# Performance work log

Measured on AMD Instinct MI355X. Metric: run time of the kernel, lower is better.

The kernel has to match this reference:

```python
import jax, jax.numpy as jnp
import numpy as np

B, T, C, HS = 4, 4096, 1024, 128

def setup_inputs() -> dict:
    key = jax.random.key(0)
    kx, kk, kq, kv = jax.random.split(key, 4)
    x = jax.random.normal(kx, (B, T, C), dtype=jnp.float32)
    # torch Linear(n_embd, head_size, bias=False): y = x @ W.T with W [hs, C].
    # We store the transposed form W [C, hs] so y = x @ W (same math).
    s = C ** -0.5  # kaiming-ish scale to keep activations sane
    Wk = jax.random.normal(kk, (C, HS), dtype=jnp.float32) * s
    Wq = jax.random.normal(kq, (C, HS), dtype=jnp.float32) * s
    Wv = jax.random.normal(kv, (C, HS), dtype=jnp.float32) * s
    return {"x": x, "Wk": Wk, "Wq": Wq, "Wv": Wv}

def reference(x, Wk, Wq, Wv):
    # Single causal self-attention head (dropout = identity, eval mode).
    k = jnp.einsum('btc,ch->bth', x, Wk)  # [B,T,hs]
    q = jnp.einsum('btc,ch->bth', x, Wq)
    v = jnp.einsum('btc,ch->bth', x, Wv)
    scale = k.shape[-1] ** -0.5
    wei = jnp.einsum('bqh,bkh->bqk', q, k) * scale  # [B,T,T]
    Tq = x.shape[1]
    causal = jnp.tril(jnp.ones((Tq, Tq), dtype=bool))
    wei = jnp.where(causal, wei, -jnp.inf)
    wei = jax.nn.softmax(wei, axis=-1)
    out = jnp.einsum('bqk,bkh->bqh', wei, v)  # [B,T,hs]
    return out
```

## Files before the change

kernel.cpp:

```cpp
#include <hip/hip_runtime.h>
#include <hip/hip_bf16.h>
#include <math.h>

#define B_  4
#define T_  4096
#define C_  1024
#define HS_ 128

using bf16x8 = __attribute__((ext_vector_type(8))) __bf16;
using bf16x4 = __attribute__((ext_vector_type(4))) __bf16;
using f32x4  = __attribute__((ext_vector_type(4))) float;

#define MFMA(a, b, c) __builtin_amdgcn_mfma_f32_16x16x32_bf16(a, b, c, 0, 0, 0)

typedef __attribute__((address_space(1))) const float gfloat;
typedef __attribute__((address_space(3))) float lfloat;

__device__ inline float fexp2(float x) {
  float r;
  asm volatile("v_exp_f32 %0, %1\n\ts_nop 0" : "=v"(r) : "v"(x));
  return r;
}


__global__ __launch_bounds__(256) void prep_w_kernel(
    const float* __restrict__ Wk, const float* __restrict__ Wq,
    const float* __restrict__ Wv, __bf16* __restrict__ Wt) {
  const int m  = blockIdx.x >> 4;
  const int k0 = (blockIdx.x & 15) * 64;
  const float* W = (m == 0) ? Wq : ((m == 1) ? Wk : Wv);
  const float scale = (m == 0) ? (0.08838834764831845f * 1.4426950408889634f) : 1.0f;
  __shared__ __bf16 tile[128][72];
  const int t = threadIdx.x;
#pragma unroll
  for (int p = 0; p < 8; ++p) {
    int e  = p * 1024 + t * 4;
    int r  = e >> 7;
    int cc = e & 127;
    float4 w = *reinterpret_cast<const float4*>(&W[(size_t)(k0 + r) * HS_ + cc]);
    tile[cc + 0][r] = (__bf16)(w.x * scale);
    tile[cc + 1][r] = (__bf16)(w.y * scale);
    tile[cc + 2][r] = (__bf16)(w.z * scale);
    tile[cc + 3][r] = (__bf16)(w.w * scale);
  }
  __syncthreads();
#pragma unroll
  for (int p = 0; p < 4; ++p) {
    int e  = p * 2048 + t * 8;
    int n  = e >> 6;
    int kk = e & 63;
    bf16x8 v;
#pragma unroll
    for (int jj = 0; jj < 8; ++jj) v[jj] = tile[n][kk + jj];
    *reinterpret_cast<bf16x8*>(&Wt[((size_t)m * 128 + n) * C_ + k0 + kk]) = v;
  }
}

__device__ inline bf16x8 cvt8p(float4 u, float4 v) {
  bf16x8 r;
  r[0] = (__bf16)u.x; r[1] = (__bf16)u.y; r[2] = (__bf16)u.z; r[3] = (__bf16)u.w;
  r[4] = (__bf16)v.x; r[5] = (__bf16)v.y; r[6] = (__bf16)v.z; r[7] = (__bf16)v.w;
  return r;
}

__global__ __launch_bounds__(256) void proj_kernel(
    const float* __restrict__ x, const __bf16* __restrict__ Wt,
    __bf16* __restrict__ Qf, __bf16* __restrict__ Kf, __bf16* __restrict__ Vf) {
  __shared__ __align__(16) char lds[57344];
  const int tid = threadIdx.x;
  const int wid = tid >> 6;
  const int l   = tid & 63;
  const int c   = l & 15;
  const int g   = l >> 4;
  const int rbase = blockIdx.x * 32;

  f32x4 acc[6][2];
#pragma unroll
  for (int i = 0; i < 6; ++i) { acc[i][0] = 0.f; acc[i][1] = 0.f; }

  const int xrow = tid >> 3;
  const int xch  = tid & 7;
  const float* xsrc = x + (size_t)(rbase + xrow) * C_ + ((xch ^ (xrow & 7)) << 2);
  const __bf16* wsrc[6];
#pragma unroll
  for (int i = 0; i < 6; ++i) {
    int id2 = i * 256 + tid;
    int cg  = id2 >> 2;
    int kc  = id2 & 3;
    wsrc[i] = Wt + (size_t)cg * C_ + ((kc ^ (cg & 3)) << 3);
  }

  auto stage = [&](int t, int bo) {
    __builtin_amdgcn_global_load_lds((gfloat*)(xsrc + t * 32),
        (lfloat*)(lds + bo + tid * 16), 16, 0, 0);
#pragma unroll
    for (int i = 0; i < 6; ++i)
      __builtin_amdgcn_global_load_lds((gfloat*)(wsrc[i] + t * 32),
          (lfloat*)(lds + bo + 4096 + (i * 256 + tid) * 16), 16, 0, 0);
  };

  int woffs[6];
#pragma unroll
  for (int i = 0; i < 6; ++i) {
    int u  = wid * 6 + i;
    int cg = (u >> 3) * 128 + (u & 7) * 16 + c;
    woffs[i] = 4096 + cg * 64 + ((g ^ (cg & 3)) << 4);
  }
  int xoffs[2][2];
#pragma unroll
  for (int rt = 0; rt < 2; ++rt) {
    int row = rt * 16 + c;
#pragma unroll
    for (int j = 0; j < 2; ++j)
      xoffs[rt][j] = row * 128 + ((((g << 1) | j) ^ (row & 7)) << 4);
  }

  stage(0, 0);
  asm volatile("s_waitcnt vmcnt(0)" ::: "memory");
  __syncthreads();

  for (int t = 0; t < 32; ++t) {
    const int bo = (t & 1) * 28672;
    if (t + 1 < 32) stage(t + 1, bo ^ 28672);

    bf16x8 wf[6];
#pragma unroll
    for (int i = 0; i < 6; ++i)
      wf[i] = *reinterpret_cast<const bf16x8*>(lds + bo + woffs[i]);
#pragma unroll
    for (int rt = 0; rt < 2; ++rt) {
      float4 lo = *reinterpret_cast<const float4*>(lds + bo + xoffs[rt][0]);
      float4 hi = *reinterpret_cast<const float4*>(lds + bo + xoffs[rt][1]);
      bf16x8 a = cvt8p(lo, hi);
#pragma unroll
      for (int i = 0; i < 6; ++i) acc[i][rt] = MFMA(a, wf[i], acc[i][rt]);
    }

    asm volatile("s_waitcnt vmcnt(0)" ::: "memory");
    __syncthreads();
  }

  const size_t tile = blockIdx.x;
#pragma unroll
  for (int i = 0; i < 6; ++i) {
    const int u = wid * 6 + i;
    const int m = u >> 3, nt = u & 7;
    const int gprime = ((nt & 1) << 1) + (c >> 3);
    const int e = c & 7;
    if (m == 0) {
#pragma unroll
      for (int rt = 0; rt < 2; ++rt)
#pragma unroll
        for (int rr = 0; rr < 4; ++rr)
          Qf[(tile * 8 + rt * 4 + (nt >> 1)) * 512 +
             (gprime * 16 + 4 * g + rr) * 8 + e] = (__bf16)acc[i][rt][rr];
    } else if (m == 1) {
#pragma unroll
      for (int rt = 0; rt < 2; ++rt)
#pragma unroll
        for (int rr = 0; rr < 4; ++rr)
          Kf[(tile * 8 + 2 * (nt >> 1) + (g & 1)) * 512 +
             (gprime * 16 + (((2 * rt + (g >> 1)) << 2) | rr)) * 8 + e] =
              (__bf16)acc[i][rt][rr];
    } else {
#pragma unroll
      for (int rt = 0; rt < 2; ++rt) {
        bf16x4 v4;
#pragma unroll
        for (int rr = 0; rr < 4; ++rr) v4[rr] = (__bf16)acc[i][rt][rr];
        *reinterpret_cast<bf16x4*>(
            Vf + (tile * 8 + nt) * 512 +
            ((2 * rt + (g >> 1)) * 16 + c) * 8 + 4 * (g & 1)) = v4;
      }
    }
  }
}

__global__ __launch_bounds__(256, 2) void attn_kernel(
    const __bf16* __restrict__ Qf, const __bf16* __restrict__ Kf,
    const __bf16* __restrict__ Vf, float* __restrict__ out) {
  __shared__ float sm[4][32];
  __shared__ float sl[4][32];
  __shared__ float bufA[32][132];
  __shared__ float bufB[32][132];

  const int tid = threadIdx.x;
  const int wid = tid >> 6;
  const int l   = tid & 63;
  const int c   = l & 15;
  const int g   = l >> 4;
  const int bid = blockIdx.x;
  const int b   = (bid & 7) >> 1;
  const int j   = ((bid >> 3) << 1) | (bid & 1);
  const int qt  = (j < 64) ? (127 - j) : (j - 64);
  const int qb  = qt * 32;

  bf16x8 qf[2][4];
  {
    const __bf16* Qt = Qf + (size_t)(b * 128 + qt) * 4096 + l * 8;
#pragma unroll
    for (int rt = 0; rt < 2; ++rt)
#pragma unroll
      for (int cs = 0; cs < 4; ++cs)
        qf[rt][cs] = *reinterpret_cast<const bf16x8*>(Qt + (rt * 4 + cs) * 512);
  }

  f32x4 acc[2][8];
#pragma unroll
  for (int i = 0; i < 2; ++i)
#pragma unroll
    for (int d = 0; d < 8; ++d) acc[i][d] = 0.f;
  float mrun[2] = {-INFINITY, -INFINITY};
  float lrun[2] = {0.f, 0.f};

  if (wid <= qt) {
    const __bf16* Kb8 = Kf + (size_t)b * 128 * 4096 + l * 8;
    const __bf16* Vb8 = Vf + (size_t)b * 128 * 4096 + l * 8;
    bf16x8 kreg[8];
    auto kload = [&](int kt) {
      const __bf16* kb = Kb8 + (size_t)kt * 4096;
#pragma unroll
      for (int jj = 0; jj < 8; ++jj)
        kreg[jj] = *reinterpret_cast<const bf16x8*>(kb + jj * 512);
    };
    kload(wid);

    for (int kt = wid; kt <= qt; kt += 4) {
      f32x4 s00 = 0.f, s01 = 0.f, s10 = 0.f, s11 = 0.f;
      __builtin_amdgcn_s_setprio(1);
#pragma unroll
      for (int cs = 0; cs < 4; ++cs) {
        s00 = MFMA(kreg[2 * cs], qf[0][cs], s00);
        s01 = MFMA(kreg[2 * cs + 1], qf[0][cs], s01);
        s10 = MFMA(kreg[2 * cs], qf[1][cs], s10);
        s11 = MFMA(kreg[2 * cs + 1], qf[1][cs], s11);
      }
      __builtin_amdgcn_s_setprio(0);

      bf16x8 vf[8];
      {
        const __bf16* vb = Vb8 + (size_t)kt * 4096;
#pragma unroll
        for (int db = 0; db < 8; ++db)
          vf[db] = *reinterpret_cast<const bf16x8*>(vb + db * 512);
      }

      if (kt + 4 <= qt) kload(kt + 4);

      const bool maskt = (kt == qt);
      bf16x8 pb[2];
#pragma unroll
      for (int rt = 0; rt < 2; ++rt) {
        float p[8];
        const f32x4 sa = rt ? s10 : s00;
        const f32x4 sb = rt ? s11 : s01;
#pragma unroll
        for (int rr = 0; rr < 4; ++rr) { p[rr] = sa[rr]; p[4 + rr] = sb[rr]; }
        if (maskt) {
          const int lim = rt * 16 + c;
#pragma unroll
          for (int jj = 0; jj < 8; ++jj)
            if (8 * g + jj > lim) p[jj] = -INFINITY;
        }
        float t0 = fmaxf(fmaxf(p[0], p[1]), p[2]);
        float t1 = fmaxf(fmaxf(p[3], p[4]), p[5]);
        float t2 = fmaxf(fmaxf(p[6], p[7]), t0);
        float tmax = fmaxf(t1, t2);

        if (!__all(tmax <= mrun[rt] + 11.5415603f)) {
          float cmax = fmaxf(tmax, __shfl_xor(tmax, 16));
          cmax = fmaxf(cmax, __shfl_xor(cmax, 32));
          float mnew = fmaxf(mrun[rt], cmax);
          float al   = fexp2(mrun[rt] - mnew);
          mrun[rt] = mnew;
          lrun[rt] *= al;
#pragma unroll
          for (int db = 0; db < 8; ++db) acc[rt][db] *= al;
        }
        const float mc = mrun[rt];
#pragma unroll
        for (int jj = 0; jj < 8; ++jj) p[jj] = fexp2(p[jj] - mc);
        lrun[rt] += ((p[0] + p[1]) + (p[2] + p[3])) + ((p[4] + p[5]) + (p[6] + p[7]));
#pragma unroll
        for (int jj = 0; jj < 8; ++jj) pb[rt][jj] = (__bf16)p[jj];
      }

      __builtin_amdgcn_s_setprio(1);
#pragma unroll
      for (int db = 0; db < 8; ++db) {
        acc[0][db] = MFMA(vf[db], pb[0], acc[0][db]);
        acc[1][db] = MFMA(vf[db], pb[1], acc[1][db]);
      }
      __builtin_amdgcn_s_setprio(0);
    }
  }

#pragma unroll
  for (int rt = 0; rt < 2; ++rt) {
    lrun[rt] += __shfl_xor(lrun[rt], 16);
    lrun[rt] += __shfl_xor(lrun[rt], 32);
  }

  if (g == 0) {
    sm[wid][c] = mrun[0]; sm[wid][16 + c] = mrun[1];
    sl[wid][c] = lrun[0]; sl[wid][16 + c] = lrun[1];
  }
  __syncthreads();

  float linv[2];
#pragma unroll
  for (int rt = 0; rt < 2; ++rt) {
    const int q = rt * 16 + c;
    float ms = fmaxf(fmaxf(sm[0][q], sm[1][q]), fmaxf(sm[2][q], sm[3][q]));
    float ls = fexp2(sm[0][q] - ms) * sl[0][q] + fexp2(sm[1][q] - ms) * sl[1][q]
             + fexp2(sm[2][q] - ms) * sl[2][q] + fexp2(sm[3][q] - ms) * sl[3][q];
    float al = fexp2(mrun[rt] - ms);
#pragma unroll
    for (int db = 0; db < 8; ++db) acc[rt][db] *= al;
    linv[rt] = 1.0f / ls;
  }

  auto store_buf = [&](float(*buf)[132]) {
#pragma unroll
    for (int rt = 0; rt < 2; ++rt)
#pragma unroll
      for (int db = 0; db < 8; ++db)
        *reinterpret_cast<f32x4*>(&buf[rt * 16 + c][db * 16 + 4 * g]) = acc[rt][db];
  };
  auto add_buf = [&](float(*buf)[132]) {
#pragma unroll
    for (int rt = 0; rt < 2; ++rt)
#pragma unroll
      for (int db = 0; db < 8; ++db)
        acc[rt][db] += *reinterpret_cast<const f32x4*>(&buf[rt * 16 + c][db * 16 + 4 * g]);
  };

  if (wid == 2) store_buf(bufA);
  if (wid == 3) store_buf(bufB);
  __syncthreads();
  if (wid == 0) add_buf(bufA);
  if (wid == 1) add_buf(bufB);
  __syncthreads();
  if (wid == 1) store_buf(bufA);
  __syncthreads();
  if (wid == 0) {
    add_buf(bufA);
    float* op = out + ((size_t)b * T_ + qb) * HS_;
#pragma unroll
    for (int rt = 0; rt < 2; ++rt)
#pragma unroll
      for (int db = 0; db < 8; ++db) {
        f32x4 v = acc[rt][db] * linv[rt];
        *reinterpret_cast<f32x4*>(op + (size_t)(rt * 16 + c) * HS_ + db * 16 + 4 * g) = v;
      }
  }
}

extern "C" void kernel_launch(void* const* d_in, const int* in_sizes, int n_in,
                              void* d_out, int out_size, void* d_ws, size_t ws_size,
                              hipStream_t stream) {
  const float* x  = (const float*)d_in[0];
  const float* Wk = (const float*)d_in[1];
  const float* Wq = (const float*)d_in[2];
  const float* Wv = (const float*)d_in[3];
  float* out = (float*)d_out;

  char* ws = (char*)d_ws;
  __bf16* Wt = (__bf16*)ws;
  __bf16* Qf = (__bf16*)(ws + 786432);
  __bf16* Kf = (__bf16*)(ws + 786432 + 4194304);
  __bf16* Vf = (__bf16*)(ws + 786432 + 8388608);

  prep_w_kernel<<<48, 256, 0, stream>>>(Wk, Wq, Wv, Wt);
  proj_kernel<<<512, 256, 0, stream>>>(x, Wt, Qf, Kf, Vf);
  attn_kernel<<<512, 256, 0, stream>>>(Qf, Kf, Vf, out);
}
```

Before: 72.42 us.

## Pre-swizzle weights into MFMA fragment order and load projection operands directly to registers

The weight-prep kernel now writes the bf16 weights in a fragment-major layout that matches the MFMA B-operand. The projection kernel drops its LDS double buffer and barriers and loads x and W fragments straight from global memory into registers, prefetching one k-step ahead. This removes LDS traffic and block-level synchronisation. In exchange each wave reads x rows redundantly from global or L2, and register pressure rises from holding the prefetched fragments.

```diff
diff --git a/kernel.cpp b/kernel.cpp
--- a/kernel.cpp
+++ b/kernel.cpp
@@ -13,9 +13,6 @@
 
 #define MFMA(a, b, c) __builtin_amdgcn_mfma_f32_16x16x32_bf16(a, b, c, 0, 0, 0)
 
-typedef __attribute__((address_space(1))) const float gfloat;
-typedef __attribute__((address_space(3))) float lfloat;
-
 __device__ inline float fexp2(float x) {
   float r;
   asm volatile("v_exp_f32 %0, %1\n\ts_nop 0" : "=v"(r) : "v"(x));
@@ -25,7 +22,7 @@
 
 __global__ __launch_bounds__(256) void prep_w_kernel(
     const float* __restrict__ Wk, const float* __restrict__ Wq,
-    const float* __restrict__ Wv, __bf16* __restrict__ Wt) {
+    const float* __restrict__ Wv, __bf16* __restrict__ Wf) {
   const int m  = blockIdx.x >> 4;
   const int k0 = (blockIdx.x & 15) * 64;
   const float* W = (m == 0) ? Wq : ((m == 1) ? Wk : Wv);
@@ -52,7 +49,11 @@
     bf16x8 v;
 #pragma unroll
     for (int jj = 0; jj < 8; ++jj) v[jj] = tile[n][kk + jj];
-    *reinterpret_cast<bf16x8*>(&Wt[((size_t)m * 128 + n) * C_ + k0 + kk]) = v;
+    int u  = m * 8 + (n >> 4);
+    int ts = (k0 + kk) >> 5;
+    int g2 = (kk >> 3) & 3;
+    *reinterpret_cast<bf16x8*>(
+        &Wf[((size_t)(u * 32 + ts) * 64 + g2 * 16 + (n & 15)) * 8]) = v;
   }
 }
 
@@ -64,9 +65,8 @@
 }
 
 __global__ __launch_bounds__(256) void proj_kernel(
-    const float* __restrict__ x, const __bf16* __restrict__ Wt,
+    const float* __restrict__ x, const __bf16* __restrict__ Wf,
     __bf16* __restrict__ Qf, __bf16* __restrict__ Kf, __bf16* __restrict__ Vf) {
-  __shared__ __align__(16) char lds[57344];
   const int tid = threadIdx.x;
   const int wid = tid >> 6;
   const int l   = tid & 63;
@@ -78,66 +78,45 @@
 #pragma unroll
   for (int i = 0; i < 6; ++i) { acc[i][0] = 0.f; acc[i][1] = 0.f; }
 
-  const int xrow = tid >> 3;
-  const int xch  = tid & 7;
-  const float* xsrc = x + (size_t)(rbase + xrow) * C_ + ((xch ^ (xrow & 7)) << 2);
-  const __bf16* wsrc[6];
-#pragma unroll
-  for (int i = 0; i < 6; ++i) {
-    int id2 = i * 256 + tid;
-    int cg  = id2 >> 2;
-    int kc  = id2 & 3;
-    wsrc[i] = Wt + (size_t)cg * C_ + ((kc ^ (cg & 3)) << 3);
-  }
-
-  auto stage = [&](int t, int bo) {
-    __builtin_amdgcn_global_load_lds((gfloat*)(xsrc + t * 32),
-        (lfloat*)(lds + bo + tid * 16), 16, 0, 0);
+  const float*  xb = x + (size_t)(rbase + c) * C_ + g * 8;
+  const __bf16* wb = Wf + (size_t)(wid * 6) * 16384 + l * 8;
+
+  float4 xc[4], xn[4];
+  bf16x8 wc[6], wn[6];
+
+  auto xload = [&](float4* d, int t) {
+    const float* p0 = xb + t * 32;
+    d[0] = *reinterpret_cast<const float4*>(p0);
+    d[1] = *reinterpret_cast<const float4*>(p0 + 4);
+    d[2] = *reinterpret_cast<const float4*>(p0 + 16 * C_);
+    d[3] = *reinterpret_cast<const float4*>(p0 + 16 * C_ + 4);
+  };
+  auto wload = [&](bf16x8* d, int t) {
 #pragma unroll
     for (int i = 0; i < 6; ++i)
-      __builtin_amdgcn_global_load_lds((gfloat*)(wsrc[i] + t * 32),
-          (lfloat*)(lds + bo + 4096 + (i * 256 + tid) * 16), 16, 0, 0);
+      d[i] = *reinterpret_cast<const bf16x8*>(wb + i * 16384 + t * 512);
   };
 
-  int woffs[6];
-#pragma unroll
-  for (int i = 0; i < 6; ++i) {
-    int u  = wid * 6 + i;
-    int cg = (u >> 3) * 128 + (u & 7) * 16 + c;
-    woffs[i] = 4096 + cg * 64 + ((g ^ (cg & 3)) << 4);
-  }
-  int xoffs[2][2];
-#pragma unroll
-  for (int rt = 0; rt < 2; ++rt) {
-    int row = rt * 16 + c;
-#pragma unroll
-    for (int j = 0; j < 2; ++j)
-      xoffs[rt][j] = row * 128 + ((((g << 1) | j) ^ (row & 7)) << 4);
-  }
-
-  stage(0, 0);
-  asm volatile("s_waitcnt vmcnt(0)" ::: "memory");
-  __syncthreads();
+  xload(xc, 0);
+  wload(wc, 0);
 
   for (int t = 0; t < 32; ++t) {
-    const int bo = (t & 1) * 28672;
-    if (t + 1 < 32) stage(t + 1, bo ^ 28672);
-
-    bf16x8 wf[6];
-#pragma unroll
-    for (int i = 0; i < 6; ++i)
-      wf[i] = *reinterpret_cast<const bf16x8*>(lds + bo + woffs[i]);
-#pragma unroll
-    for (int rt = 0; rt < 2; ++rt) {
-      float4 lo = *reinterpret_cast<const float4*>(lds + bo + xoffs[rt][0]);
-      float4 hi = *reinterpret_cast<const float4*>(lds + bo + xoffs[rt][1]);
-      bf16x8 a = cvt8p(lo, hi);
-#pragma unroll
-      for (int i = 0; i < 6; ++i) acc[i][rt] = MFMA(a, wf[i], acc[i][rt]);
+    if (t + 1 < 32) { xload(xn, t + 1); wload(wn, t + 1); }
+
+    bf16x8 a0 = cvt8p(xc[0], xc[1]);
+    bf16x8 a1 = cvt8p(xc[2], xc[3]);
+#pragma unroll
+    for (int i = 0; i < 6; ++i) {
+      acc[i][0] = MFMA(a0, wc[i], acc[i][0]);
+      acc[i][1] = MFMA(a1, wc[i], acc[i][1]);
     }
 
-    asm volatile("s_waitcnt vmcnt(0)" ::: "memory");
-    __syncthreads();
+    if (t + 1 < 32) {
+#pragma unroll
+      for (int j = 0; j < 4; ++j) xc[j] = xn[j];
+#pragma unroll
+      for (int i = 0; i < 6; ++i) wc[i] = wn[i];
+    }
   }
 
   const size_t tile = blockIdx.x;
@@ -366,12 +345,12 @@
   float* out = (float*)d_out;
 
   char* ws = (char*)d_ws;
-  __bf16* Wt = (__bf16*)ws;
+  __bf16* Wf = (__bf16*)ws;
   __bf16* Qf = (__bf16*)(ws + 786432);
   __bf16* Kf = (__bf16*)(ws + 786432 + 4194304);
   __bf16* Vf = (__bf16*)(ws + 786432 + 8388608);
 
-  prep_w_kernel<<<48, 256, 0, stream>>>(Wk, Wq, Wv, Wt);
-  proj_kernel<<<512, 256, 0, stream>>>(x, Wt, Qf, Kf, Vf);
+  prep_w_kernel<<<48, 256, 0, stream>>>(Wk, Wq, Wv, Wf);
+  proj_kernel<<<512, 256, 0, stream>>>(x, Wf, Qf, Kf, Vf);
   attn_kernel<<<512, 256, 0, stream>>>(Qf, Kf, Vf, out);
 }
```

Measured after the change: 77.90 us. 1.08x slower.

## Pre-swizzle weights into MFMA fragment layout and double proj block to 512 threads

Applied to the files above, without the earlier changes.

The weight prep kernel now writes bf16 weights directly in per-tile MFMA fragment order, so each 32-wide k-step of a 16-column tile is one contiguous 1KB chunk. The projection kernel uses 512 threads (8 waves), each wave handling 3 output tiles instead of 6. This halves per-wave accumulators and loads and makes weight staging fully contiguous, with no XOR swizzle. The x tile is staged by only the first 256 threads. The aim is more waves to hide latency and simpler, coalesced weight loads, at the cost of reading the shared x fragment twice as many times across waves.

```diff
diff --git a/kernel.cpp b/kernel.cpp
--- a/kernel.cpp
+++ b/kernel.cpp
@@ -25,7 +25,7 @@
 
 __global__ __launch_bounds__(256) void prep_w_kernel(
     const float* __restrict__ Wk, const float* __restrict__ Wq,
-    const float* __restrict__ Wv, __bf16* __restrict__ Wt) {
+    const float* __restrict__ Wv, __bf16* __restrict__ Wf) {
   const int m  = blockIdx.x >> 4;
   const int k0 = (blockIdx.x & 15) * 64;
   const float* W = (m == 0) ? Wq : ((m == 1) ? Wk : Wv);
@@ -52,7 +52,11 @@
     bf16x8 v;
 #pragma unroll
     for (int jj = 0; jj < 8; ++jj) v[jj] = tile[n][kk + jj];
-    *reinterpret_cast<bf16x8*>(&Wt[((size_t)m * 128 + n) * C_ + k0 + kk]) = v;
+    int u  = m * 8 + (n >> 4);
+    int ts = (k0 + kk) >> 5;
+    int g2 = (kk >> 3) & 3;
+    *reinterpret_cast<bf16x8*>(
+        &Wf[((size_t)(u * 32 + ts) * 64 + g2 * 16 + (n & 15)) * 8]) = v;
   }
 }
 
@@ -63,8 +67,8 @@
   return r;
 }
 
-__global__ __launch_bounds__(256) void proj_kernel(
-    const float* __restrict__ x, const __bf16* __restrict__ Wt,
+__global__ __launch_bounds__(512) void proj_kernel(
+    const float* __restrict__ x, const __bf16* __restrict__ Wf,
     __bf16* __restrict__ Qf, __bf16* __restrict__ Kf, __bf16* __restrict__ Vf) {
   __shared__ __align__(16) char lds[57344];
   const int tid = threadIdx.x;
@@ -74,38 +78,38 @@
   const int g   = l >> 4;
   const int rbase = blockIdx.x * 32;
 
-  f32x4 acc[6][2];
-#pragma unroll
-  for (int i = 0; i < 6; ++i) { acc[i][0] = 0.f; acc[i][1] = 0.f; }
-
-  const int xrow = tid >> 3;
+  f32x4 acc[3][2];
+#pragma unroll
+  for (int i = 0; i < 3; ++i) { acc[i][0] = 0.f; acc[i][1] = 0.f; }
+
+  const int xrow = (tid & 255) >> 3;
   const int xch  = tid & 7;
   const float* xsrc = x + (size_t)(rbase + xrow) * C_ + ((xch ^ (xrow & 7)) << 2);
-  const __bf16* wsrc[6];
-#pragma unroll
-  for (int i = 0; i < 6; ++i) {
-    int id2 = i * 256 + tid;
-    int cg  = id2 >> 2;
-    int kc  = id2 & 3;
-    wsrc[i] = Wt + (size_t)cg * C_ + ((kc ^ (cg & 3)) << 3);
+  const __bf16* wsrc[3];
+  int wdst[3];
+#pragma unroll
+  for (int i = 0; i < 3; ++i) {
+    int id = i * 512 + tid;
+    int u  = id >> 6;
+    int ln = id & 63;
+    wsrc[i] = Wf + (size_t)u * 32 * 512 + ln * 8;
+    wdst[i] = 4096 + id * 16;
   }
 
   auto stage = [&](int t, int bo) {
-    __builtin_amdgcn_global_load_lds((gfloat*)(xsrc + t * 32),
-        (lfloat*)(lds + bo + tid * 16), 16, 0, 0);
-#pragma unroll
-    for (int i = 0; i < 6; ++i)
-      __builtin_amdgcn_global_load_lds((gfloat*)(wsrc[i] + t * 32),
-          (lfloat*)(lds + bo + 4096 + (i * 256 + tid) * 16), 16, 0, 0);
+    if (tid < 256)
+      __builtin_amdgcn_global_load_lds((gfloat*)(xsrc + t * 32),
+          (lfloat*)(lds + bo + tid * 16), 16, 0, 0);
+#pragma unroll
+    for (int i = 0; i < 3; ++i)
+      __builtin_amdgcn_global_load_lds((gfloat*)(wsrc[i] + t * 512),
+          (lfloat*)(lds + bo + wdst[i]), 16, 0, 0);
   };
 
-  int woffs[6];
-#pragma unroll
-  for (int i = 0; i < 6; ++i) {
-    int u  = wid * 6 + i;
-    int cg = (u >> 3) * 128 + (u & 7) * 16 + c;
-    woffs[i] = 4096 + cg * 64 + ((g ^ (cg & 3)) << 4);
-  }
+  int woffs[3];
+#pragma unroll
+  for (int i = 0; i < 3; ++i)
+    woffs[i] = 4096 + (wid * 3 + i) * 1024 + l * 16;
   int xoffs[2][2];
 #pragma unroll
   for (int rt = 0; rt < 2; ++rt) {
@@ -123,9 +127,9 @@
     const int bo = (t & 1) * 28672;
     if (t + 1 < 32) stage(t + 1, bo ^ 28672);
 
-    bf16x8 wf[6];
-#pragma unroll
-    for (int i = 0; i < 6; ++i)
+    bf16x8 wf[3];
+#pragma unroll
+    for (int i = 0; i < 3; ++i)
       wf[i] = *reinterpret_cast<const bf16x8*>(lds + bo + woffs[i]);
 #pragma unroll
     for (int rt = 0; rt < 2; ++rt) {
@@ -133,7 +137,7 @@
       float4 hi = *reinterpret_cast<const float4*>(lds + bo + xoffs[rt][1]);
       bf16x8 a = cvt8p(lo, hi);
 #pragma unroll
-      for (int i = 0; i < 6; ++i) acc[i][rt] = MFMA(a, wf[i], acc[i][rt]);
+      for (int i = 0; i < 3; ++i) acc[i][rt] = MFMA(a, wf[i], acc[i][rt]);
     }
 
     asm volatile("s_waitcnt vmcnt(0)" ::: "memory");
@@ -142,8 +146,8 @@
 
   const size_t tile = blockIdx.x;
 #pragma unroll
-  for (int i = 0; i < 6; ++i) {
-    const int u = wid * 6 + i;
+  for (int i = 0; i < 3; ++i) {
+    const int u = wid * 3 + i;
     const int m = u >> 3, nt = u & 7;
     const int gprime = ((nt & 1) << 1) + (c >> 3);
     const int e = c & 7;
@@ -366,12 +370,12 @@
   float* out = (float*)d_out;
 
   char* ws = (char*)d_ws;
-  __bf16* Wt = (__bf16*)ws;
+  __bf16* Wf = (__bf16*)ws;
   __bf16* Qf = (__bf16*)(ws + 786432);
   __bf16* Kf = (__bf16*)(ws + 786432 + 4194304);
   __bf16* Vf = (__bf16*)(ws + 786432 + 8388608);
 
-  prep_w_kernel<<<48, 256, 0, stream>>>(Wk, Wq, Wv, Wt);
-  proj_kernel<<<512, 256, 0, stream>>>(x, Wt, Qf, Kf, Vf);
+  prep_w_kernel<<<48, 256, 0, stream>>>(Wk, Wq, Wv, Wf);
+  proj_kernel<<<512, 512, 0, stream>>>(x, Wf, Qf, Kf, Vf);
   attn_kernel<<<512, 256, 0, stream>>>(Qf, Kf, Vf, out);
 }
```

Result: faster. 64.77 us (-10.6%).
